# Kernel tuning notes

Measured on AMD Instinct MI355X. Metric: run time of the kernel, lower is better.

Reference implementation:

```python
import jax, jax.numpy as jnp
import numpy as np

B, S, D = 8, 1024, 1024
H, DH = 16, 64  # num_attention_heads, attention_head_size; H*DH == D


def setup_inputs() -> dict:
    key = jax.random.key(0)
    ks = jax.random.split(key, 6)
    scale = 0.02
    return {
        "hidden_states": jax.random.normal(ks[0], (B, S, D), jnp.float32),
        "right_hidden_states": jax.random.normal(ks[1], (B, S, D), jnp.float32),
        "attention_mask": jnp.ones((B, S, S), jnp.float32),
        "Wq": jax.random.normal(ks[2], (D, H * DH), jnp.float32) * scale,
        "bq": jnp.zeros((H * DH,), jnp.float32),
        "Wk": jax.random.normal(ks[3], (D, H * DH), jnp.float32) * scale,
        "bk": jnp.zeros((H * DH,), jnp.float32),
        "Wv": jax.random.normal(ks[4], (D, H * DH), jnp.float32) * scale,
        "bv": jnp.zeros((H * DH,), jnp.float32),
    }


def _split_heads(x, b):
    # (B, S, H*DH) -> (B, H, S, DH)
    return x.reshape(b, -1, H, DH).transpose(0, 2, 1, 3)


def reference(hidden_states, right_hidden_states, attention_mask, Wq, bq, Wk, bk, Wv, bv):
    b = hidden_states.shape[0]
    q = _split_heads(hidden_states @ Wq + bq, b)          # (B,H,Sq,DH)
    k = _split_heads(right_hidden_states @ Wk + bk, b)    # (B,H,Sk,DH)
    v = _split_heads(right_hidden_states @ Wv + bv, b)    # (B,H,Sk,DH)

    scores = jnp.einsum("bhqd,bhkd->bhqk", q, k) / jnp.sqrt(jnp.asarray(DH, q.dtype))
    scores = jnp.sum(scores, axis=1, keepdims=True)       # (B,1,Sq,Sk) head-summed

    ext = (1.0 - attention_mask[:, None, :, :].astype(scores.dtype)) * -1e9
    probs = jax.nn.softmax(scores + ext, axis=-1)         # (B,1,Sq,Sk)

    ctx = jnp.matmul(probs, v)                            # broadcast -> (B,H,Sq,DH)
    # Faithful to original: reshape WITHOUT transposing heads back.
    return ctx.reshape(b, -1, H * DH)                     # (B,Sq,H*DH)
```

## Files before the change

kernel.cpp:

```cpp
#include <hip/hip_runtime.h>
#include <stdint.h>

constexpr int S = 1024;
constexpr int D = 1024;
constexpr int NB = 8;

typedef __bf16 bf16x8 __attribute__((ext_vector_type(8)));
typedef float floatx4 __attribute__((ext_vector_type(4)));

#define AS1 __attribute__((address_space(1)))
#define AS3 __attribute__((address_space(3)))

__device__ __forceinline__ unsigned short f2bf(float f) {
  unsigned u = __builtin_bit_cast(unsigned, f);
  u += 0x7fffu + ((u >> 16) & 1u);
  return (unsigned short)(u >> 16);
}

__device__ __forceinline__ void gload16(const void* g, void* l) {
  __builtin_amdgcn_global_load_lds((const AS1 unsigned int*)g, (AS3 unsigned int*)l, 16, 0, 0);
}

__global__ __launch_bounds__(256) void prep_kernel(const float4* __restrict__ hs4,
                                                   const float4* __restrict__ rhs4,
                                                   ushort4* __restrict__ hsb4,
                                                   ushort4* __restrict__ rhsb4, int n4,
                                                   const float* __restrict__ Wq,
                                                   const float* __restrict__ Wk,
                                                   const float* __restrict__ Wv,
                                                   unsigned short* __restrict__ Wcat) {
  __shared__ float tile[32][33];
  const int bid = blockIdx.x;
  if (bid < 16384) {
    int i = bid * 256 + threadIdx.x;
    const float4* src;
    ushort4* dst;
    int j;
    if (i < n4) {
      src = hs4; dst = hsb4; j = i;
    } else {
      src = rhs4; dst = rhsb4; j = i - n4;
    }
    float4 v = src[j];
    ushort4 o;
    o.x = f2bf(v.x); o.y = f2bf(v.y); o.z = f2bf(v.z); o.w = f2bf(v.w);
    dst[j] = o;
  } else {
    const int t = bid - 16384;
    const int z = t >> 10;
    const int r = t & 1023;
    const float* W = (z == 0) ? Wq : (z == 1) ? Wk : Wv;
    unsigned short* Wt = Wcat + (long long)z * D * D;
    const int bx = (r & 31) * 32;
    const int by = (r >> 5) * 32;
    const int x = threadIdx.x & 31;
    const int y0 = threadIdx.x >> 5;
    for (int i = 0; i < 4; ++i) {
      int y = y0 + i * 8;
      tile[y][x] = W[(by + y) * D + bx + x];
    }
    __syncthreads();
    for (int i = 0; i < 4; ++i) {
      int y = y0 + i * 8;
      Wt[(long long)(bx + y) * D + by + x] = f2bf(tile[x][y]);
    }
  }
}


#define GEMM_STAGE_SETUP(Abase, lda_, Bbase, ldb_)                            \
  const int srow = tid >> 2;                                                  \
  const int scg = (((tid & 3) ^ ((srow >> 1) & 3)) * 8);                      \
  const unsigned short* aG0 = (Abase) + (long long)srow * (lda_) + scg;       \
  const unsigned short* aG1 = aG0 + (long long)64 * (lda_);                   \
  const unsigned short* bG0 = (Bbase) + (long long)srow * (ldb_) + scg;       \
  const unsigned short* bG1 = bG0 + (long long)64 * (ldb_);

#define GEMM_KLOOP(Klen)                                                                 \
  for (int k0 = 0; k0 < (Klen); k0 += 64) {                                              \
    gload16(aG0 + k0, As[0] + w * 512);                                                  \
    gload16(aG1 + k0, As[0] + w * 512 + 2048);                                           \
    gload16(aG0 + k0 + 32, As[1] + w * 512);                                             \
    gload16(aG1 + k0 + 32, As[1] + w * 512 + 2048);                                      \
    gload16(bG0 + k0, Bs[0] + w * 512);                                                  \
    gload16(bG1 + k0, Bs[0] + w * 512 + 2048);                                           \
    gload16(bG0 + k0 + 32, Bs[1] + w * 512);                                             \
    gload16(bG1 + k0 + 32, Bs[1] + w * 512 + 2048);                                      \
    __syncthreads();                                                                     \
    for (int h = 0; h < 2; ++h) {                                                        \
      bf16x8 af[4], bfr[4];                                                              \
      for (int t = 0; t < 4; ++t) {                                                      \
        af[t] = *reinterpret_cast<const bf16x8*>(As[h] + (wm + t * 16 + r15) * 32 + pq); \
        bfr[t] = *reinterpret_cast<const bf16x8*>(Bs[h] + (wn + t * 16 + r15) * 32 + pq);\
      }                                                                                  \
      for (int mt = 0; mt < 4; ++mt)                                                     \
        for (int nt = 0; nt < 4; ++nt)                                                   \
          acc[mt][nt] =                                                                  \
              __builtin_amdgcn_mfma_f32_16x16x32_bf16(af[mt], bfr[nt], acc[mt][nt], 0, 0, 0); \
    }                                                                                    \
    __syncthreads();                                                                     \
  }

#define GEMM_COMMON_IDX                  \
  const int tid = threadIdx.x;           \
  const int lane = tid & 63;             \
  const int w = tid >> 6;                \
  const int r15 = lane & 15;             \
  const int quad = lane >> 4;            \
  const int pq = (quad ^ ((r15 >> 1) & 3)) * 8; \
  const int wm = (w >> 1) * 64;          \
  const int wn = (w & 1) * 64;

#define GEMM_ACC_INIT                    \
  floatx4 acc[4][4];                     \
  for (int i = 0; i < 4; ++i)            \
    for (int j = 0; j < 4; ++j) acc[i][j] = {0.f, 0.f, 0.f, 0.f};

__global__ __launch_bounds__(256) void gemm_qkv_kernel(
    const unsigned short* __restrict__ hsb, const unsigned short* __restrict__ rhsb,
    const unsigned short* __restrict__ Wcat, unsigned short* __restrict__ Qm,
    unsigned short* __restrict__ Km, unsigned short* __restrict__ Vmt,
    const float* __restrict__ bq, const float* __restrict__ bk, const float* __restrict__ bv) {
  __shared__ __align__(16) unsigned short As[2][4096];
  __shared__ __align__(16) unsigned short Bs[2][4096];
  GEMM_COMMON_IDX
  const int bid = blockIdx.x;
  const int swz = (bid & 7) * 192 + (bid >> 3);
  const int bx = swz % 24;
  const int by = swz / 24;
  const long long n0g = (long long)bx * 128;
  const int seg = (int)(n0g >> 10);
  const long long m0 = (long long)by * 128;
  const unsigned short* A = ((seg == 0) ? hsb : rhsb) + m0 * D;
  const unsigned short* Bt = Wcat + n0g * D;
  const float* bias = (seg == 0) ? bq : (seg == 1) ? bk : bv;

  GEMM_STAGE_SETUP(A, D, Bt, D)
  GEMM_ACC_INIT
  GEMM_KLOOP(D)

  const long long nloc0 = n0g & 1023;
  for (int mt = 0; mt < 4; ++mt) {
    for (int nt = 0; nt < 4; ++nt) {
      const long long mrow = m0 + wm + mt * 16 + quad * 4;
      const long long nc = nloc0 + wn + nt * 16 + r15;
      const float bval = bias[nc];
      floatx4 v = acc[mt][nt];
      for (int e = 0; e < 4; ++e) {
        float val = v[e] + bval;
        long long m = mrow + e;
        if (seg == 0) {
          Qm[m * D + nc] = f2bf(val);
        } else if (seg == 1) {
          Km[m * D + nc] = f2bf(val);
        } else {
          Vmt[(m >> 10) * (long long)(S * D) + nc * S + (m & 1023)] = f2bf(val);
        }
      }
    }
  }
}

__global__ __launch_bounds__(256) void gemm_scores_kernel(
    const unsigned short* __restrict__ Qm, const unsigned short* __restrict__ Km,
    const float* __restrict__ mask, unsigned short* __restrict__ E,
    float* __restrict__ rowsumP) {
  __shared__ __align__(16) unsigned short As[2][4096];
  __shared__ __align__(16) unsigned short Bs[2][4096];
  GEMM_COMMON_IDX
  const int bid = blockIdx.x;
  const int z = bid & 7;
  const int r = bid >> 3;
  const int bx = r & 7;
  const int by = r >> 3;
  const long long m0 = (long long)by * 128;
  const long long n0 = (long long)bx * 128;
  const unsigned short* A = Qm + (long long)z * S * D + m0 * D;
  const unsigned short* Bt = Km + (long long)z * S * D + n0 * D;

  GEMM_STAGE_SETUP(A, D, Bt, D)
  GEMM_ACC_INIT
  GEMM_KLOOP(D)

  const long long zE = (long long)z * S * 1024;
  float rowpart[4][4];
  for (int mt = 0; mt < 4; ++mt)
    for (int e = 0; e < 4; ++e) rowpart[mt][e] = 0.f;

  for (int mt = 0; mt < 4; ++mt) {
    for (int nt = 0; nt < 4; ++nt) {
      const long long mrow = m0 + wm + mt * 16 + quad * 4;
      const long long nc = n0 + wn + nt * 16 + r15;
      floatx4 v = acc[mt][nt];
      for (int e = 0; e < 4; ++e) {
        long long m = mrow + e;
        float mval = mask[zE + m * 1024 + nc];
        float sc = v[e] * 0.125f + (1.0f - mval) * -1e9f;
        float Ev = __expf(sc);
        E[zE + m * 1024 + nc] = f2bf(Ev);
        rowpart[mt][e] += Ev;
      }
    }
  }
  const int slot = (bx << 11) + ((wn >> 6) << 10);
  for (int mt = 0; mt < 4; ++mt) {
    for (int e = 0; e < 4; ++e) {
      float s = rowpart[mt][e];
      s += __shfl_xor(s, 1, 64);
      s += __shfl_xor(s, 2, 64);
      s += __shfl_xor(s, 4, 64);
      s += __shfl_xor(s, 8, 64);
      if (r15 == 0) {
        int mloc = (int)(m0 + wm + mt * 16 + quad * 4 + e);
        rowsumP[(z << 14) + slot + mloc] = s;
      }
    }
  }
}

__global__ __launch_bounds__(256) void gemm_ctx_kernel(const unsigned short* __restrict__ E,
                                                       const unsigned short* __restrict__ Vmt,
                                                       const float* __restrict__ rowsumP,
                                                       float* __restrict__ out) {
  __shared__ __align__(16) unsigned short As[2][4096];
  __shared__ __align__(16) unsigned short Bs[2][4096];
  __shared__ float rsinv[128];
  GEMM_COMMON_IDX
  const int bid = blockIdx.x;
  const int z = bid & 7;
  const int r = bid >> 3;
  const int bx = r & 7;
  const int by = r >> 3;
  const long long m0 = (long long)by * 128;
  const long long n0 = (long long)bx * 128;
  const unsigned short* A = E + (long long)z * S * 1024 + m0 * 1024;
  const unsigned short* Bt = Vmt + (long long)z * S * D + n0 * D;

  if (tid < 128) {
    float s = 0.f;
    for (int t = 0; t < 16; ++t) s += rowsumP[(z << 14) + (t << 10) + (int)m0 + tid];
    rsinv[tid] = 1.0f / s;
  }

  GEMM_STAGE_SETUP(A, 1024, Bt, D)
  GEMM_ACC_INIT
  GEMM_KLOOP(1024)

  for (int mt = 0; mt < 4; ++mt) {
    for (int nt = 0; nt < 4; ++nt) {
      const int r0 = wm + mt * 16 + quad * 4;
      const long long ncol = n0 + wn + nt * 16 + r15;
      floatx4 v = acc[mt][nt];
      for (int e = 0; e < 4; ++e) {
        long long m = m0 + r0 + e;
        float val = v[e] * rsinv[r0 + e];
        out[(long long)z * S * D + (ncol >> 6) * (long long)(S * 64) + m * 64 + (ncol & 63)] =
            val;
      }
    }
  }
}

extern "C" void kernel_launch(void* const* d_in, const int* in_sizes, int n_in, void* d_out,
                              int out_size, void* d_ws, size_t ws_size, hipStream_t stream) {
  const float* hs = (const float*)d_in[0];
  const float* rhs = (const float*)d_in[1];
  const float* mask = (const float*)d_in[2];
  const float* Wq = (const float*)d_in[3];
  const float* bq = (const float*)d_in[4];
  const float* Wk = (const float*)d_in[5];
  const float* bk = (const float*)d_in[6];
  const float* Wv = (const float*)d_in[7];
  const float* bv = (const float*)d_in[8];
  float* out = (float*)d_out;
  char* ws = (char*)d_ws;
  const size_t MB = 1ull << 20;
  unsigned short* Wcat = (unsigned short*)(ws + 0 * MB);
  unsigned short* hsb = (unsigned short*)(ws + 6 * MB);
  unsigned short* rhsb = (unsigned short*)(ws + 22 * MB);
  unsigned short* Qm = (unsigned short*)(ws + 38 * MB);
  unsigned short* Km = (unsigned short*)(ws + 54 * MB);
  unsigned short* Vmt = (unsigned short*)(ws + 70 * MB);
  unsigned short* E = (unsigned short*)(ws + 6 * MB);
  float* rowsumP = (float*)(ws + 22 * MB);

  const int n4 = NB * S * D / 4;
  prep_kernel<<<16384 + 3072, 256, 0, stream>>>((const float4*)hs, (const float4*)rhs,
                                                (ushort4*)hsb, (ushort4*)rhsb, n4, Wq, Wk, Wv,
                                                Wcat);

  gemm_qkv_kernel<<<dim3(1536), 256, 0, stream>>>(hsb, rhsb, Wcat, Qm, Km, Vmt, bq, bk, bv);

  gemm_scores_kernel<<<dim3(512), 256, 0, stream>>>(Qm, Km, mask, E, rowsumP);

  gemm_ctx_kernel<<<dim3(512), 256, 0, stream>>>(E, Vmt, rowsumP, out);
}
```

Measured before the change: 291.7 us.

## Use 256x128 tiles with 8 waves and double-buffered LDS prefetch in GEMMs

Rewrites the shared GEMM mainloop used by the QKV, scores and context kernels. Tiles grow to 256x128, blocks grow to 512 threads (8 waves), and LDS becomes double-buffered so the next k-tile is loaded with global_load_lds while MFMAs run on the current one. It also adds explicit barriers, waitcnt and setprio around MFMA groups. Grids shrink by half, so fewer blocks are available to fill the CUs, and the hand-tuned waitcnt/barrier ordering risks subtle hazards.

```diff
diff --git a/kernel.cpp b/kernel.cpp
--- a/kernel.cpp
+++ b/kernel.cpp
@@ -68,84 +68,133 @@
 }
 
 
-#define GEMM_STAGE_SETUP(Abase, lda_, Bbase, ldb_)                            \
-  const int srow = tid >> 2;                                                  \
-  const int scg = (((tid & 3) ^ ((srow >> 1) & 3)) * 8);                      \
-  const unsigned short* aG0 = (Abase) + (long long)srow * (lda_) + scg;       \
-  const unsigned short* aG1 = aG0 + (long long)64 * (lda_);                   \
-  const unsigned short* bG0 = (Bbase) + (long long)srow * (ldb_) + scg;       \
-  const unsigned short* bG1 = bG0 + (long long)64 * (ldb_);
-
-#define GEMM_KLOOP(Klen)                                                                 \
-  for (int k0 = 0; k0 < (Klen); k0 += 64) {                                              \
-    gload16(aG0 + k0, As[0] + w * 512);                                                  \
-    gload16(aG1 + k0, As[0] + w * 512 + 2048);                                           \
-    gload16(aG0 + k0 + 32, As[1] + w * 512);                                             \
-    gload16(aG1 + k0 + 32, As[1] + w * 512 + 2048);                                      \
-    gload16(bG0 + k0, Bs[0] + w * 512);                                                  \
-    gload16(bG1 + k0, Bs[0] + w * 512 + 2048);                                           \
-    gload16(bG0 + k0 + 32, Bs[1] + w * 512);                                             \
-    gload16(bG1 + k0 + 32, Bs[1] + w * 512 + 2048);                                      \
-    __syncthreads();                                                                     \
-    for (int h = 0; h < 2; ++h) {                                                        \
-      bf16x8 af[4], bfr[4];                                                              \
-      for (int t = 0; t < 4; ++t) {                                                      \
-        af[t] = *reinterpret_cast<const bf16x8*>(As[h] + (wm + t * 16 + r15) * 32 + pq); \
-        bfr[t] = *reinterpret_cast<const bf16x8*>(Bs[h] + (wn + t * 16 + r15) * 32 + pq);\
-      }                                                                                  \
-      for (int mt = 0; mt < 4; ++mt)                                                     \
-        for (int nt = 0; nt < 4; ++nt)                                                   \
-          acc[mt][nt] =                                                                  \
-              __builtin_amdgcn_mfma_f32_16x16x32_bf16(af[mt], bfr[nt], acc[mt][nt], 0, 0, 0); \
-    }                                                                                    \
-    __syncthreads();                                                                     \
-  }
-
-#define GEMM_COMMON_IDX                  \
-  const int tid = threadIdx.x;           \
-  const int lane = tid & 63;             \
-  const int w = tid >> 6;                \
-  const int r15 = lane & 15;             \
-  const int quad = lane >> 4;            \
-  const int pq = (quad ^ ((r15 >> 1) & 3)) * 8; \
-  const int wm = (w >> 1) * 64;          \
-  const int wn = (w & 1) * 64;
-
-#define GEMM_ACC_INIT                    \
-  floatx4 acc[4][4];                     \
-  for (int i = 0; i < 4; ++i)            \
-    for (int j = 0; j < 4; ++j) acc[i][j] = {0.f, 0.f, 0.f, 0.f};
-
-__global__ __launch_bounds__(256) void gemm_qkv_kernel(
+#define G8_IDX                                   \
+  const int tid = threadIdx.x;                   \
+  const int lane = tid & 63;                     \
+  const int w = tid >> 6;                        \
+  const int wr = w >> 2;                         \
+  const int wc = w & 3;                          \
+  const int r15 = lane & 15;                     \
+  const int quad = lane >> 4;                    \
+  const int pq = (quad ^ ((r15 >> 1) & 3)) * 8;  \
+  const int srow = tid >> 2;                     \
+  const int scg = (((tid & 3) ^ ((srow >> 1) & 3)) * 8);
+
+#define G8_STAGE_SETUP(Abase, lda_, Bbase, ldb_)                        \
+  const unsigned short* aG = (Abase) + (long long)srow * (lda_) + scg;  \
+  const long long aR2 = (long long)128 * (lda_);                        \
+  const unsigned short* bG = (Bbase) + (long long)srow * (ldb_) + scg;
+
+#define G8_STAGE_A(BUF, kk, ko)                                                       \
+  gload16(aG + (ko) + (kk) * 32, Sh + (BUF) * 24576 + (kk) * 8192 + w * 512);         \
+  gload16(aG + (ko) + (kk) * 32 + aR2, Sh + (BUF) * 24576 + (kk) * 8192 + w * 512 + 4096);
+#define G8_STAGE_B(BUF, kk, ko)                                                       \
+  gload16(bG + (ko) + (kk) * 32, Sh + (BUF) * 24576 + 16384 + (kk) * 4096 + w * 512);
+
+#define G8_LDA(BUF, kk, row) \
+  (*reinterpret_cast<const bf16x8*>(Sh + (BUF) * 24576 + (kk) * 8192 + (row) * 32 + pq))
+#define G8_LDB(BUF, kk, row) \
+  (*reinterpret_cast<const bf16x8*>(Sh + (BUF) * 24576 + 16384 + (kk) * 4096 + (row) * 32 + pq))
+
+#define G8_MFMA8(ACCOFF, AFR, BFR)                                              \
+  __builtin_amdgcn_s_setprio(1);                                                \
+  _Pragma("unroll") for (int mf = 0; mf < 4; ++mf)                              \
+  _Pragma("unroll") for (int nf = 0; nf < 2; ++nf)                              \
+      acc[(ACCOFF) + mf][nf] = __builtin_amdgcn_mfma_f32_16x16x32_bf16(         \
+          AFR[mf], BFR[nf], acc[(ACCOFF) + mf][nf], 0, 0, 0);                   \
+  __builtin_amdgcn_s_setprio(0);
+
+#define G8_TILE(CUR, T)                                                         \
+  {                                                                             \
+    const int tn_ = ((T) + 1 < 16) ? (T) + 1 : (T);                             \
+    const long long knx_ = (long long)tn_ * 64;                                 \
+    bf16x8 a_[4], b0_[2], b1_[2];                                               \
+                              \
+    _Pragma("unroll") for (int mf = 0; mf < 4; ++mf)                            \
+        a_[mf] = G8_LDA(CUR, 0, wr * 128 + mf * 16 + r15);                      \
+    _Pragma("unroll") for (int nf = 0; nf < 2; ++nf)                            \
+        b0_[nf] = G8_LDB(CUR, 0, wc * 32 + nf * 16 + r15);                      \
+    G8_STAGE_A((CUR) ^ 1, 0, knx_)                                              \
+    __builtin_amdgcn_s_barrier();                                               \
+    asm volatile("s_waitcnt lgkmcnt(0)" ::: "memory");                          \
+    G8_MFMA8(0, a_, b0_)                                                        \
+    __builtin_amdgcn_s_barrier();                                               \
+                          \
+    _Pragma("unroll") for (int mf = 0; mf < 4; ++mf)                            \
+        a_[mf] = G8_LDA(CUR, 0, wr * 128 + 64 + mf * 16 + r15);                 \
+    G8_STAGE_B((CUR) ^ 1, 0, knx_)                                              \
+    asm volatile("s_waitcnt vmcnt(3)" ::: "memory");                            \
+    __builtin_amdgcn_s_barrier();                                               \
+    asm volatile("s_waitcnt lgkmcnt(0)" ::: "memory");                          \
+    G8_MFMA8(4, a_, b0_)                                                        \
+    __builtin_amdgcn_s_barrier();                                               \
+                              \
+    _Pragma("unroll") for (int mf = 0; mf < 4; ++mf)                            \
+        a_[mf] = G8_LDA(CUR, 1, wr * 128 + mf * 16 + r15);                      \
+    _Pragma("unroll") for (int nf = 0; nf < 2; ++nf)                            \
+        b1_[nf] = G8_LDB(CUR, 1, wc * 32 + nf * 16 + r15);                      \
+    G8_STAGE_A((CUR) ^ 1, 1, knx_)                                              \
+    __builtin_amdgcn_s_barrier();                                               \
+    asm volatile("s_waitcnt lgkmcnt(0)" ::: "memory");                          \
+    G8_MFMA8(0, a_, b1_)                                                        \
+    __builtin_amdgcn_s_barrier();                                               \
+                          \
+    _Pragma("unroll") for (int mf = 0; mf < 4; ++mf)                            \
+        a_[mf] = G8_LDA(CUR, 1, wr * 128 + 64 + mf * 16 + r15);                 \
+    G8_STAGE_B((CUR) ^ 1, 1, knx_)                                              \
+    asm volatile("s_waitcnt vmcnt(3)" ::: "memory");                            \
+    __builtin_amdgcn_s_barrier();                                               \
+    asm volatile("s_waitcnt lgkmcnt(0)" ::: "memory");                          \
+    G8_MFMA8(4, a_, b1_)                                                        \
+    __builtin_amdgcn_s_barrier();                                               \
+  }
+
+#define G8_KLOOP                                       \
+  G8_STAGE_A(0, 0, 0)                                  \
+  G8_STAGE_B(0, 0, 0)                                  \
+  G8_STAGE_A(0, 1, 0)                                  \
+  G8_STAGE_B(0, 1, 0)                                  \
+  asm volatile("s_waitcnt vmcnt(3)" ::: "memory");     \
+  __builtin_amdgcn_s_barrier();                        \
+  for (int t = 0; t < 16; t += 2) {                    \
+    G8_TILE(0, t)                                      \
+    G8_TILE(1, t + 1)                                  \
+  }
+
+#define G8_ACC_INIT                    \
+  floatx4 acc[8][2];                   \
+  _Pragma("unroll") for (int i = 0; i < 8; ++i)        \
+  _Pragma("unroll") for (int j = 0; j < 2; ++j) acc[i][j] = {0.f, 0.f, 0.f, 0.f};
+
+__global__ __launch_bounds__(512, 2) void gemm_qkv_kernel(
     const unsigned short* __restrict__ hsb, const unsigned short* __restrict__ rhsb,
     const unsigned short* __restrict__ Wcat, unsigned short* __restrict__ Qm,
     unsigned short* __restrict__ Km, unsigned short* __restrict__ Vmt,
     const float* __restrict__ bq, const float* __restrict__ bk, const float* __restrict__ bv) {
-  __shared__ __align__(16) unsigned short As[2][4096];
-  __shared__ __align__(16) unsigned short Bs[2][4096];
-  GEMM_COMMON_IDX
+  __shared__ __align__(16) unsigned short Sh[49152];
+  G8_IDX
   const int bid = blockIdx.x;
-  const int swz = (bid & 7) * 192 + (bid >> 3);
+  const int swz = (bid & 7) * 96 + (bid >> 3);
   const int bx = swz % 24;
   const int by = swz / 24;
   const long long n0g = (long long)bx * 128;
-  const int seg = (int)(n0g >> 10);
-  const long long m0 = (long long)by * 128;
+  const int seg = bx >> 3;
+  const long long m0 = (long long)by * 256;
   const unsigned short* A = ((seg == 0) ? hsb : rhsb) + m0 * D;
   const unsigned short* Bt = Wcat + n0g * D;
   const float* bias = (seg == 0) ? bq : (seg == 1) ? bk : bv;
 
-  GEMM_STAGE_SETUP(A, D, Bt, D)
-  GEMM_ACC_INIT
-  GEMM_KLOOP(D)
+  G8_STAGE_SETUP(A, D, Bt, D)
+  G8_ACC_INIT
+  G8_KLOOP
 
   const long long nloc0 = n0g & 1023;
-  for (int mt = 0; mt < 4; ++mt) {
-    for (int nt = 0; nt < 4; ++nt) {
-      const long long mrow = m0 + wm + mt * 16 + quad * 4;
-      const long long nc = nloc0 + wn + nt * 16 + r15;
+  for (int i = 0; i < 8; ++i) {
+    for (int nf = 0; nf < 2; ++nf) {
+      const long long mrow = m0 + wr * 128 + i * 16 + quad * 4;
+      const long long nc = nloc0 + wc * 32 + nf * 16 + r15;
       const float bval = bias[nc];
-      floatx4 v = acc[mt][nt];
+      floatx4 v = acc[i][nf];
       for (int e = 0; e < 4; ++e) {
         float val = v[e] + bval;
         long long m = mrow + e;
@@ -161,96 +210,95 @@
   }
 }
 
-__global__ __launch_bounds__(256) void gemm_scores_kernel(
+__global__ __launch_bounds__(512, 2) void gemm_scores_kernel(
     const unsigned short* __restrict__ Qm, const unsigned short* __restrict__ Km,
     const float* __restrict__ mask, unsigned short* __restrict__ E,
     float* __restrict__ rowsumP) {
-  __shared__ __align__(16) unsigned short As[2][4096];
-  __shared__ __align__(16) unsigned short Bs[2][4096];
-  GEMM_COMMON_IDX
+  __shared__ __align__(16) unsigned short Sh[49152];
+  G8_IDX
   const int bid = blockIdx.x;
   const int z = bid & 7;
   const int r = bid >> 3;
+  const int by = r >> 3;
   const int bx = r & 7;
-  const int by = r >> 3;
-  const long long m0 = (long long)by * 128;
+  const long long m0 = (long long)by * 256;
   const long long n0 = (long long)bx * 128;
   const unsigned short* A = Qm + (long long)z * S * D + m0 * D;
   const unsigned short* Bt = Km + (long long)z * S * D + n0 * D;
 
-  GEMM_STAGE_SETUP(A, D, Bt, D)
-  GEMM_ACC_INIT
-  GEMM_KLOOP(D)
+  G8_STAGE_SETUP(A, D, Bt, D)
+  G8_ACC_INIT
+  G8_KLOOP
 
   const long long zE = (long long)z * S * 1024;
-  float rowpart[4][4];
-  for (int mt = 0; mt < 4; ++mt)
-    for (int e = 0; e < 4; ++e) rowpart[mt][e] = 0.f;
-
-  for (int mt = 0; mt < 4; ++mt) {
-    for (int nt = 0; nt < 4; ++nt) {
-      const long long mrow = m0 + wm + mt * 16 + quad * 4;
-      const long long nc = n0 + wn + nt * 16 + r15;
-      floatx4 v = acc[mt][nt];
+  float rowpart[8][4];
+  for (int i = 0; i < 8; ++i)
+    for (int e = 0; e < 4; ++e) rowpart[i][e] = 0.f;
+
+  for (int i = 0; i < 8; ++i) {
+    for (int nf = 0; nf < 2; ++nf) {
+      const long long mrow = m0 + wr * 128 + i * 16 + quad * 4;
+      const long long nc = n0 + wc * 32 + nf * 16 + r15;
+      floatx4 v = acc[i][nf];
       for (int e = 0; e < 4; ++e) {
         long long m = mrow + e;
         float mval = mask[zE + m * 1024 + nc];
         float sc = v[e] * 0.125f + (1.0f - mval) * -1e9f;
         float Ev = __expf(sc);
         E[zE + m * 1024 + nc] = f2bf(Ev);
-        rowpart[mt][e] += Ev;
+        rowpart[i][e] += Ev;
       }
     }
   }
-  const int slot = (bx << 11) + ((wn >> 6) << 10);
-  for (int mt = 0; mt < 4; ++mt) {
+  const int slot = bx * 4 + wc;
+  for (int i = 0; i < 8; ++i) {
     for (int e = 0; e < 4; ++e) {
-      float s = rowpart[mt][e];
+      float s = rowpart[i][e];
       s += __shfl_xor(s, 1, 64);
       s += __shfl_xor(s, 2, 64);
       s += __shfl_xor(s, 4, 64);
       s += __shfl_xor(s, 8, 64);
       if (r15 == 0) {
-        int mloc = (int)(m0 + wm + mt * 16 + quad * 4 + e);
-        rowsumP[(z << 14) + slot + mloc] = s;
+        int mloc = (int)(m0 + wr * 128 + i * 16 + quad * 4 + e);
+        rowsumP[(z << 15) + (slot << 10) + mloc] = s;
       }
     }
   }
 }
 
-__global__ __launch_bounds__(256) void gemm_ctx_kernel(const unsigned short* __restrict__ E,
-                                                       const unsigned short* __restrict__ Vmt,
-                                                       const float* __restrict__ rowsumP,
-                                                       float* __restrict__ out) {
-  __shared__ __align__(16) unsigned short As[2][4096];
-  __shared__ __align__(16) unsigned short Bs[2][4096];
-  __shared__ float rsinv[128];
-  GEMM_COMMON_IDX
+__global__ __launch_bounds__(512, 2) void gemm_ctx_kernel(const unsigned short* __restrict__ E,
+                                                          const unsigned short* __restrict__ Vmt,
+                                                          const float* __restrict__ rowsumP,
+                                                          float* __restrict__ out) {
+  __shared__ __align__(16) unsigned short Sh[49152];
+  __shared__ float rsinv[256];
+  G8_IDX
   const int bid = blockIdx.x;
   const int z = bid & 7;
   const int r = bid >> 3;
+  const int by = r >> 3;
   const int bx = r & 7;
-  const int by = r >> 3;
-  const long long m0 = (long long)by * 128;
+  const long long m0 = (long long)by * 256;
   const long long n0 = (long long)bx * 128;
   const unsigned short* A = E + (long long)z * S * 1024 + m0 * 1024;
   const unsigned short* Bt = Vmt + (long long)z * S * D + n0 * D;
 
-  if (tid < 128) {
+  if (tid < 256) {
     float s = 0.f;
-    for (int t = 0; t < 16; ++t) s += rowsumP[(z << 14) + (t << 10) + (int)m0 + tid];
+    for (int t = 0; t < 32; ++t) s += rowsumP[(z << 15) + (t << 10) + (int)m0 + tid];
     rsinv[tid] = 1.0f / s;
   }
-
-  GEMM_STAGE_SETUP(A, 1024, Bt, D)
-  GEMM_ACC_INIT
-  GEMM_KLOOP(1024)
-
-  for (int mt = 0; mt < 4; ++mt) {
-    for (int nt = 0; nt < 4; ++nt) {
-      const int r0 = wm + mt * 16 + quad * 4;
-      const long long ncol = n0 + wn + nt * 16 + r15;
-      floatx4 v = acc[mt][nt];
+  __syncthreads();
+
+  G8_STAGE_SETUP(A, 1024, Bt, D)
+  G8_ACC_INIT
+  G8_KLOOP
+
+  for (int i = 0; i < 8; ++i) {
+    for (int nf = 0; nf < 2; ++nf) {
+      const int r0 = wr * 128 + i * 16 + quad * 4;
+      const long long ncol = n0 + wc * 32 + nf * 16 + r15;
+      floatx4 v = acc[i][nf];
       for (int e = 0; e < 4; ++e) {
         long long m = m0 + r0 + e;
         float val = v[e] * rsinv[r0 + e];
@@ -289,9 +337,9 @@
                                                 (ushort4*)hsb, (ushort4*)rhsb, n4, Wq, Wk, Wv,
                                                 Wcat);
 
-  gemm_qkv_kernel<<<dim3(1536), 256, 0, stream>>>(hsb, rhsb, Wcat, Qm, Km, Vmt, bq, bk, bv);
-
-  gemm_scores_kernel<<<dim3(512), 256, 0, stream>>>(Qm, Km, mask, E, rowsumP);
-
-  gemm_ctx_kernel<<<dim3(512), 256, 0, stream>>>(E, Vmt, rowsumP, out);
-}
+  gemm_qkv_kernel<<<dim3(768), 512, 0, stream>>>(hsb, rhsb, Wcat, Qm, Km, Vmt, bq, bk, bv);
+
+  gemm_scores_kernel<<<dim3(256), 512, 0, stream>>>(Qm, Km, mask, E, rowsumP);
+
+  gemm_ctx_kernel<<<dim3(256), 512, 0, stream>>>(E, Vmt, rowsumP, out);
+}
```

After: 293.6 us. No clear change (+0.6%).
